# Kernel tuning notes

Measured on AMD Instinct MI355X. Metric: run time of the kernel, lower is better.

## Reference

```python
import jax, jax.numpy as jnp
import numpy as np

TEMP = 0.07
EPS = 1e-12


def _l2norm(x):
    # F.normalize(x, dim=1): divide by clamped L2 norm
    n = jnp.sqrt(jnp.sum(x * x, axis=1, keepdims=True))
    return x / jnp.maximum(n, EPS)


def _pool_cat(slow, fast):
    # AdaptiveAvgPool3d((1,1,1)) == mean over (T,H,W); concat channels -> [B, 2304]
    return jnp.concatenate([slow.mean(axis=(2, 3, 4)), fast.mean(axis=(2, 3, 4))], axis=1)


def _sim_targets(sim_labels, same_idx):
    # Vectorized replacement of the per-row python loop; targets are constants
    # (built from .item() in torch), hence stop_gradient.
    B = sim_labels.shape[0]
    eye = jnp.eye(B, dtype=sim_labels.dtype)
    pos = jnp.diagonal(sim_labels)[:, None]                    # [B,1]
    neg = (1.0 - pos) / (B - 1)
    soft = eye * pos + (1.0 - eye) * neg                       # same_idx in {1,3,4}
    uni = jnp.full((B, B), 1.0 / B, dtype=sim_labels.dtype)    # same_idx == 0
    si = same_idx[:, None]
    t = jnp.where(si == 2, eye, jnp.where(si == 0, uni, soft))
    return jax.lax.stop_gradient(t)


def setup_inputs() -> dict:
    key = jax.random.key(0)
    ks = jax.random.split(key, 16)
    B = 64
    inp = {
        "fpv_slow": jax.random.normal(ks[0], (B, 2048, 8, 7, 7), jnp.float32),
        "fpv_fast": jax.random.normal(ks[1], (B, 256, 32, 7, 7), jnp.float32),
        "tpv_slow": jax.random.normal(ks[2], (B, 2048, 8, 7, 7), jnp.float32),
        "tpv_fast": jax.random.normal(ks[3], (B, 256, 32, 7, 7), jnp.float32),
        "labels_v": jax.random.uniform(ks[4], (B, 97), jnp.float32),
        "labels_n": jax.random.uniform(ks[5], (B, 300), jnp.float32),
        "labels_v_lt": jax.random.uniform(ks[6], (B, 97), jnp.float32),
        "labels_n_lt": jax.random.uniform(ks[7], (B, 300), jnp.float32),
        "same_idx": jax.random.randint(ks[8], (B,), 0, 5, jnp.int64 if jax.config.jax_enable_x64 else jnp.int32),
        "W_fpv": jax.random.normal(ks[9], (2304, 256), jnp.float32) * 0.02,
        "b_fpv": jax.random.normal(ks[10], (256,), jnp.float32) * 0.02,
        "W_tpv": jax.random.normal(ks[11], (2304, 256), jnp.float32) * 0.02,
        "b_tpv": jax.random.normal(ks[12], (256,), jnp.float32) * 0.02,
    }
    return inp


def reference(fpv_slow, fpv_fast, tpv_slow, tpv_fast,
              labels_v, labels_n, labels_v_lt, labels_n_lt,
              same_idx, W_fpv, b_fpv, W_tpv, b_tpv):
    x_fpv = _l2norm(_pool_cat(fpv_slow, fpv_fast))             # [B,2304]
    x_tpv = _l2norm(_pool_cat(tpv_slow, tpv_fast))
    f = _l2norm(x_fpv @ W_fpv + b_fpv)                         # [B,256]
    t = _l2norm(x_tpv @ W_tpv + b_tpv)
    sim_preds = (f @ t.T) / TEMP                               # [B,B]
    sim_labels = (labels_v @ labels_v_lt.T + labels_n @ labels_n_lt.T) * 0.5
    targets = _sim_targets(sim_labels, same_idx)
    loss = -jnp.sum(jax.nn.log_softmax(sim_preds, axis=1) * targets, axis=1).mean()
    return loss
```

## Files before the change

### kernel.cpp

```cpp
#include <hip/hip_runtime.h>
#include <math.h>

#define TEMP 0.07f
#define EPSN 1e-12f

__device__ __forceinline__ float wave_reduce_sum(float v) {
    #pragma unroll
    for (int off = 32; off > 0; off >>= 1)
        v += __shfl_xor(v, off, 64);
    return v;
}

__device__ __forceinline__ float wave_reduce_max(float v) {
    #pragma unroll
    for (int off = 32; off > 0; off >>= 1)
        v = fmaxf(v, __shfl_xor(v, off, 64));
    return v;
}

__global__ __launch_bounds__(256) void pool_kernel(
    const float* __restrict__ fpv_slow, const float* __restrict__ fpv_fast,
    const float* __restrict__ tpv_slow, const float* __restrict__ tpv_fast,
    float* __restrict__ pool )
{
    const int wave = (int)((blockIdx.x * blockDim.x + threadIdx.x) >> 6);
    const int lane = threadIdx.x & 63;

    if (wave < 2 * 131072) {
        const int tensor = wave >> 17;
        const int row    = wave & 131071;
        const float* src = tensor ? tpv_slow : fpv_slow;
        const float4* p  = (const float4*)src + (size_t)row * 98;
        float4 a = p[lane];
        float s = a.x + a.y + a.z + a.w;
        if (lane < 34) {
            float4 c4 = p[64 + lane];
            s += c4.x + c4.y + c4.z + c4.w;
        }
        s = wave_reduce_sum(s);
        if (lane == 0) {
            const int b = row >> 11, c = row & 2047;
            pool[tensor * (64 * 2304) + b * 2304 + c] = s * (1.0f / 392.0f);
        }
    } else {
        const int w2     = wave - 2 * 131072;
        const int tensor = w2 >> 14;
        const int row    = w2 & 16383;
        const float* src = tensor ? tpv_fast : fpv_fast;
        const float4* p  = (const float4*)src + (size_t)row * 392;
        float s = 0.0f;
        #pragma unroll 2
        for (int i = lane; i < 392; i += 64) {
            float4 a = p[i];
            s += a.x + a.y + a.z + a.w;
        }
        s = wave_reduce_sum(s);
        if (lane == 0) {
            const int b = row >> 8, c = row & 255;
            pool[tensor * (64 * 2304) + b * 2304 + 2048 + c] = s * (1.0f / 1568.0f);
        }
    }
}

__global__ __launch_bounds__(256) void head_kernel(
    const float* __restrict__ pool,
    const float* __restrict__ W_f, const float* __restrict__ b_f,
    const float* __restrict__ W_t, const float* __restrict__ b_t,
    float* __restrict__ ft )
{
    __shared__ float xs[2304];
    __shared__ float partial[4][256];
    __shared__ float red[8];

    const int tid  = threadIdx.x;
    const int wv   = tid >> 6, lane = tid & 63;
    const int h    = blockIdx.x >> 6, b = blockIdx.x & 63;
    const float* W    = h ? W_t : W_f;
    const float* bias = h ? b_t : b_f;
    const float* xrow = pool + h * (64 * 2304) + b * 2304;

    float ss = 0.0f;
    #pragma unroll
    for (int r = 0; r < 9; ++r) {
        const int k = tid + r * 256;
        const float v = xrow[k];
        xs[k] = v;
        ss += v * v;
    }
    ss = wave_reduce_sum(ss);
    if (lane == 0) red[wv] = ss;
    __syncthreads();
    const float scale1 = 1.0f / fmaxf(sqrtf(red[0] + red[1] + red[2] + red[3]), EPSN);

    float4 acc = make_float4(0.f, 0.f, 0.f, 0.f);
    const int k0 = wv * 576;
    const float4* Wv = (const float4*)W;
    #pragma unroll 4
    for (int k = 0; k < 576; ++k) {
        const float xk = xs[k0 + k];
        const float4 w4 = Wv[(size_t)(k0 + k) * 64 + lane];
        acc.x += xk * w4.x; acc.y += xk * w4.y;
        acc.z += xk * w4.z; acc.w += xk * w4.w;
    }
    *(float4*)&partial[wv][4 * lane] = acc;
    __syncthreads();

    float y = partial[0][tid] + partial[1][tid] + partial[2][tid] + partial[3][tid];
    y = y * scale1 + bias[tid];

    float ss2 = wave_reduce_sum(y * y);
    if (lane == 0) red[4 + wv] = ss2;
    __syncthreads();
    const float scale2 = 1.0f / fmaxf(sqrtf(red[4] + red[5] + red[6] + red[7]), EPSN);

    ft[h * (64 * 256) + b * 256 + tid] = y * scale2;
}

__global__ __launch_bounds__(256) void loss_kernel(
    const float* __restrict__ ft,
    const float* __restrict__ lv, const float* __restrict__ lvlt,
    const float* __restrict__ ln, const float* __restrict__ lnlt,
    const int* __restrict__ same_idx,
    float* __restrict__ out)
{
    __shared__ float fs[256];
    __shared__ float sim[64];
    __shared__ float pos_sh;

    const int i   = blockIdx.x;
    const int tid = threadIdx.x, wv = tid >> 6, lane = tid & 63;
    const float* f = ft;
    const float* t = ft + 64 * 256;

    fs[tid] = f[i * 256 + tid];
    if (wv == 3) {
        float s = 0.0f;
        for (int k = lane; k < 97; k += 64)  s += lv[i * 97 + k]  * lvlt[i * 97 + k];
        for (int k = lane; k < 300; k += 64) s += ln[i * 300 + k] * lnlt[i * 300 + k];
        s = wave_reduce_sum(s);
        if (lane == 0) pos_sh = 0.5f * s;
    }
    __syncthreads();

    const float4 a = ((const float4*)fs)[lane];
    for (int jj = 0; jj < 16; ++jj) {
        const int j = wv * 16 + jj;
        const float4 b4 = ((const float4*)(t + j * 256))[lane];
        float d = a.x * b4.x + a.y * b4.y + a.z * b4.z + a.w * b4.w;
        d = wave_reduce_sum(d);
        if (lane == 0) sim[j] = d / TEMP;
    }
    __syncthreads();

    if (wv == 0) {
        const int si = same_idx[i];
        const float pos = pos_sh;
        const float x = sim[lane];
        const float m = wave_reduce_max(x);
        const float e = expf(x - m);
        const float s = wave_reduce_sum(e);
        const float lse = logf(s);
        float w;
        if (si == 2)      w = (lane == i) ? 1.0f : 0.0f;
        else if (si == 0) w = 1.0f / 64.0f;
        else {
            const float neg = (1.0f - pos) * (1.0f / 63.0f);
            w = (lane == i) ? pos : neg;
        }
        const float dotv = wave_reduce_sum(w * x);
        if (lane == 0) atomicAdd(out, (m + lse - dotv) * (1.0f / 64.0f));
    }
}

extern "C" void kernel_launch(void* const* d_in, const int* in_sizes, int n_in,
                              void* d_out, int out_size, void* d_ws, size_t ws_size,
                              hipStream_t stream) {
    const float* fpv_slow   = (const float*)d_in[0];
    const float* fpv_fast   = (const float*)d_in[1];
    const float* tpv_slow   = (const float*)d_in[2];
    const float* tpv_fast   = (const float*)d_in[3];
    const float* labels_v    = (const float*)d_in[4];
    const float* labels_n    = (const float*)d_in[5];
    const float* labels_v_lt = (const float*)d_in[6];
    const float* labels_n_lt = (const float*)d_in[7];
    const int*   same_idx    = (const int*)d_in[8];
    const float* W_fpv = (const float*)d_in[9];
    const float* b_fpv = (const float*)d_in[10];
    const float* W_tpv = (const float*)d_in[11];
    const float* b_tpv = (const float*)d_in[12];

    float* pool = (float*)d_ws;
    float* ft   = pool + 2 * 64 * 2304;
    float* out  = (float*)d_out;

    hipMemsetAsync(d_out, 0, sizeof(float) * out_size, stream);

    pool_kernel<<<73728, 256, 0, stream>>>(fpv_slow, fpv_fast, tpv_slow, tpv_fast, pool);
    head_kernel<<<128, 256, 0, stream>>>(pool, W_fpv, b_fpv, W_tpv, b_tpv, ft);
    loss_kernel<<<64, 256, 0, stream>>>(ft, labels_v, labels_v_lt, labels_n, labels_n_lt,
                                        same_idx, out);
}
```

Before: 607.5 us.

## Pool four slow rows per wave and split head GEMV across K-chunks

The pooling kernel now has each wave reduce four consecutive slow-path channels with all loads issued up front, and fully unrolls the fast-path loads. This cuts the wave count and raises memory-level parallelism, and the four results go out as one float4 store. The head projection is split into a 1152-block GEMV over nine K-chunks plus a finalize kernel that sums the partials and applies both normalizations. That raises parallelism for the weight streaming, which previously ran on only 128 blocks, at the cost of one extra launch and a partials buffer in workspace.

```diff
diff --git a/kernel.cpp b/kernel.cpp
--- a/kernel.cpp
+++ b/kernel.cpp
@@ -23,36 +23,63 @@
     const float* __restrict__ tpv_slow, const float* __restrict__ tpv_fast,
     float* __restrict__ pool )
 {
-    const int wave = (int)((blockIdx.x * blockDim.x + threadIdx.x) >> 6);
+    const int gw   = (int)((blockIdx.x * blockDim.x + threadIdx.x) >> 6);
     const int lane = threadIdx.x & 63;
 
-    if (wave < 2 * 131072) {
-        const int tensor = wave >> 17;
-        const int row    = wave & 131071;
+    if (gw < 65536) {
+        const int tensor = gw >> 15;
+        const int base   = (gw & 32767) * 4;
         const float* src = tensor ? tpv_slow : fpv_slow;
-        const float4* p  = (const float4*)src + (size_t)row * 98;
-        float4 a = p[lane];
-        float s = a.x + a.y + a.z + a.w;
-        if (lane < 34) {
-            float4 c4 = p[64 + lane];
-            s += c4.x + c4.y + c4.z + c4.w;
-        }
-        s = wave_reduce_sum(s);
+        const float4* p  = (const float4*)src;
+        const bool lo    = lane < 34;
+
+        const float4 a0 = p[(size_t)(base + 0) * 98 + lane];
+        const float4 a1 = p[(size_t)(base + 1) * 98 + lane];
+        const float4 a2 = p[(size_t)(base + 2) * 98 + lane];
+        const float4 a3 = p[(size_t)(base + 3) * 98 + lane];
+        float s0 = a0.x + a0.y + a0.z + a0.w;
+        float s1 = a1.x + a1.y + a1.z + a1.w;
+        float s2 = a2.x + a2.y + a2.z + a2.w;
+        float s3 = a3.x + a3.y + a3.z + a3.w;
+        if (lo) {
+            const float4 b0 = p[(size_t)(base + 0) * 98 + 64 + lane];
+            const float4 b1 = p[(size_t)(base + 1) * 98 + 64 + lane];
+            const float4 b2 = p[(size_t)(base + 2) * 98 + 64 + lane];
+            const float4 b3 = p[(size_t)(base + 3) * 98 + 64 + lane];
+            s0 += b0.x + b0.y + b0.z + b0.w;
+            s1 += b1.x + b1.y + b1.z + b1.w;
+            s2 += b2.x + b2.y + b2.z + b2.w;
+            s3 += b3.x + b3.y + b3.z + b3.w;
+        }
+        s0 = wave_reduce_sum(s0);
+        s1 = wave_reduce_sum(s1);
+        s2 = wave_reduce_sum(s2);
+        s3 = wave_reduce_sum(s3);
         if (lane == 0) {
-            const int b = row >> 11, c = row & 2047;
-            pool[tensor * (64 * 2304) + b * 2304 + c] = s * (1.0f / 392.0f);
+            const int b = base >> 11, c = base & 2047;
+            float4 o = make_float4(s0, s1, s2, s3);
+            o.x *= (1.0f / 392.0f); o.y *= (1.0f / 392.0f);
+            o.z *= (1.0f / 392.0f); o.w *= (1.0f / 392.0f);
+            *(float4*)&pool[tensor * (64 * 2304) + b * 2304 + c] = o;
         }
     } else {
-        const int w2     = wave - 2 * 131072;
+        const int w2     = gw - 65536;
         const int tensor = w2 >> 14;
         const int row    = w2 & 16383;
         const float* src = tensor ? tpv_fast : fpv_fast;
         const float4* p  = (const float4*)src + (size_t)row * 392;
-        float s = 0.0f;
-        #pragma unroll 2
-        for (int i = lane; i < 392; i += 64) {
-            float4 a = p[i];
-            s += a.x + a.y + a.z + a.w;
+        const float4 a0 = p[lane];
+        const float4 a1 = p[64 + lane];
+        const float4 a2 = p[128 + lane];
+        const float4 a3 = p[192 + lane];
+        const float4 a4 = p[256 + lane];
+        const float4 a5 = p[320 + lane];
+        float s = (a0.x + a0.y + a0.z + a0.w) + (a1.x + a1.y + a1.z + a1.w)
+                + (a2.x + a2.y + a2.z + a2.w) + (a3.x + a3.y + a3.z + a3.w)
+                + (a4.x + a4.y + a4.z + a4.w) + (a5.x + a5.y + a5.z + a5.w);
+        if (lane < 8) {
+            const float4 t = p[384 + lane];
+            s += t.x + t.y + t.z + t.w;
         }
         s = wave_reduce_sum(s);
         if (lane == 0) {
@@ -62,29 +89,54 @@
     }
 }
 
-__global__ __launch_bounds__(256) void head_kernel(
+__global__ __launch_bounds__(256) void gemv_kernel(
     const float* __restrict__ pool,
-    const float* __restrict__ W_f, const float* __restrict__ b_f,
-    const float* __restrict__ W_t, const float* __restrict__ b_t,
+    const float* __restrict__ W_f, const float* __restrict__ W_t,
+    float* __restrict__ gp )
+{
+    __shared__ float xs[256];
+    __shared__ float partial[4][256];
+
+    const int tid = threadIdx.x, wv = tid >> 6, lane = tid & 63;
+    const int idx = blockIdx.x;
+    const int ks  = idx % 9;
+    const int hb  = idx / 9;
+    const int h   = hb >> 6, b = hb & 63;
+    const float* W = h ? W_t : W_f;
+
+    xs[tid] = pool[h * (64 * 2304) + b * 2304 + ks * 256 + tid];
+    __syncthreads();
+
+    float4 acc = make_float4(0.f, 0.f, 0.f, 0.f);
+    const float4* Wv = (const float4*)W + (size_t)(ks * 256 + wv * 64) * 64 + lane;
+    #pragma unroll 8
+    for (int kk = 0; kk < 64; ++kk) {
+        const float xk = xs[wv * 64 + kk];
+        const float4 w4 = Wv[(size_t)kk * 64];
+        acc.x += xk * w4.x; acc.y += xk * w4.y;
+        acc.z += xk * w4.z; acc.w += xk * w4.w;
+    }
+    *(float4*)&partial[wv][4 * lane] = acc;
+    __syncthreads();
+
+    gp[(size_t)idx * 256 + tid] =
+        partial[0][tid] + partial[1][tid] + partial[2][tid] + partial[3][tid];
+}
+
+__global__ __launch_bounds__(256) void finalize_kernel(
+    const float* __restrict__ pool, const float* __restrict__ gp,
+    const float* __restrict__ b_f, const float* __restrict__ b_t,
     float* __restrict__ ft )
 {
-    __shared__ float xs[2304];
-    __shared__ float partial[4][256];
     __shared__ float red[8];
-
-    const int tid  = threadIdx.x;
-    const int wv   = tid >> 6, lane = tid & 63;
-    const int h    = blockIdx.x >> 6, b = blockIdx.x & 63;
-    const float* W    = h ? W_t : W_f;
-    const float* bias = h ? b_t : b_f;
+    const int tid = threadIdx.x, wv = tid >> 6, lane = tid & 63;
+    const int h = blockIdx.x >> 6, b = blockIdx.x & 63;
+
     const float* xrow = pool + h * (64 * 2304) + b * 2304;
-
     float ss = 0.0f;
     #pragma unroll
     for (int r = 0; r < 9; ++r) {
-        const int k = tid + r * 256;
-        const float v = xrow[k];
-        xs[k] = v;
+        const float v = xrow[tid + r * 256];
         ss += v * v;
     }
     ss = wave_reduce_sum(ss);
@@ -92,23 +144,14 @@
     __syncthreads();
     const float scale1 = 1.0f / fmaxf(sqrtf(red[0] + red[1] + red[2] + red[3]), EPSN);
 
-    float4 acc = make_float4(0.f, 0.f, 0.f, 0.f);
-    const int k0 = wv * 576;
-    const float4* Wv = (const float4*)W;
-    #pragma unroll 4
-    for (int k = 0; k < 576; ++k) {
-        const float xk = xs[k0 + k];
-        const float4 w4 = Wv[(size_t)(k0 + k) * 64 + lane];
-        acc.x += xk * w4.x; acc.y += xk * w4.y;
-        acc.z += xk * w4.z; acc.w += xk * w4.w;
-    }
-    *(float4*)&partial[wv][4 * lane] = acc;
-    __syncthreads();
-
-    float y = partial[0][tid] + partial[1][tid] + partial[2][tid] + partial[3][tid];
+    float y = 0.0f;
+    const float* g = gp + (size_t)(h * 64 + b) * 9 * 256;
+    #pragma unroll
+    for (int ks = 0; ks < 9; ++ks) y += g[ks * 256 + tid];
+    const float* bias = h ? b_t : b_f;
     y = y * scale1 + bias[tid];
 
-    float ss2 = wave_reduce_sum(y * y);
+    const float ss2 = wave_reduce_sum(y * y);
     if (lane == 0) red[4 + wv] = ss2;
     __syncthreads();
     const float scale2 = 1.0f / fmaxf(sqrtf(red[4] + red[5] + red[6] + red[7]), EPSN);
@@ -190,13 +233,15 @@
     const float* b_tpv = (const float*)d_in[12];
 
     float* pool = (float*)d_ws;
-    float* ft   = pool + 2 * 64 * 2304;
+    float* gp   = pool + 2 * 64 * 2304;
+    float* ft   = gp + 1152 * 256;
     float* out  = (float*)d_out;
 
     hipMemsetAsync(d_out, 0, sizeof(float) * out_size, stream);
 
-    pool_kernel<<<73728, 256, 0, stream>>>(fpv_slow, fpv_fast, tpv_slow, tpv_fast, pool);
-    head_kernel<<<128, 256, 0, stream>>>(pool, W_fpv, b_fpv, W_tpv, b_tpv, ft);
+    pool_kernel<<<24576, 256, 0, stream>>>(fpv_slow, fpv_fast, tpv_slow, tpv_fast, pool);
+    gemv_kernel<<<1152, 256, 0, stream>>>(pool, W_fpv, W_tpv, gp);
+    finalize_kernel<<<128, 256, 0, stream>>>(pool, gp, b_fpv, b_tpv, ft);
     loss_kernel<<<64, 256, 0, stream>>>(ft, labels_v, labels_v_lt, labels_n, labels_n_lt,
                                         same_idx, out);
 }
```

Result: faster. 559.1 us (-8.0%).
